# Performance work log

Hardware: AMD Instinct MI355X
Metric: run time of the kernel (lower is better)

Reference implementation:

```python
import jax, jax.numpy as jnp
import numpy as np
from jax import lax

B, D, H, FF, M = 256, 256, 8, 1024, 2048
HD = D // H
SCALE = 1.0 / np.sqrt(HD).astype(np.float32)
THR, MOM, LR = 0.5, 0.9, 0.1


def setup_inputs() -> dict:
    key = jax.random.key(0)
    ks = jax.random.split(key, 8)
    w = lambda k, sh: jax.random.normal(k, sh, dtype=jnp.float32) * 0.02
    return {
        "src": jax.random.normal(ks[0], (B, D), dtype=jnp.float32),
        "memory": jax.random.normal(ks[1], (M, D), dtype=jnp.float32) * 0.1,
        "momentum": jnp.zeros((M, D), jnp.float32),
        "scores": jax.random.uniform(ks[2], (M,), dtype=jnp.float32),
        "in_proj_w": w(ks[3], (3 * D, D)), "in_proj_b": jnp.zeros((3 * D,), jnp.float32),
        "out_w": w(ks[4], (D, D)), "out_b": jnp.zeros((D,), jnp.float32),
        "w1": w(ks[5], (FF, D)), "b1": jnp.zeros((FF,), jnp.float32),
        "w2": w(ks[6], (D, FF)), "b2": jnp.zeros((D,), jnp.float32),
        "g1": jnp.ones((D,), jnp.float32), "be1": jnp.zeros((D,), jnp.float32),
        "g2": jnp.ones((D,), jnp.float32), "be2": jnp.zeros((D,), jnp.float32),
        "ptr": M,
    }


def _ln(x, g, b):
    m = x.mean(-1, keepdims=True)
    v = ((x - m) ** 2).mean(-1, keepdims=True)
    return (x - m) / jnp.sqrt(v + 1e-5) * g + b


def reference(src, memory, momentum, scores, in_proj_w, in_proj_b, out_w, out_b,
              w1, b1, w2, b2, g1, be1, g2, be2, ptr):
    # --- surprise: 1 - max cosine similarity to memory slots ---
    xn = src / jnp.maximum(jnp.linalg.norm(src, axis=-1, keepdims=True), 1e-8)
    mn = memory / jnp.maximum(jnp.linalg.norm(memory, axis=-1, keepdims=True), 1e-8)
    sims = xn @ mn.T                                    # [B, M]
    surprises = jnp.where(jnp.linalg.norm(memory) == 0.0,
                          jnp.ones((B,), src.dtype), 1.0 - sims.max(-1))
    # --- self-attention; only the last (src) query row is used ---
    Wq, Wk, Wv = jnp.split(in_proj_w, 3, axis=0)
    bq, bk, bv = jnp.split(in_proj_b, 3, axis=0)
    q = (src @ Wq.T + bq).reshape(B, H, HD)             # [B,H,HD]
    k_mem = (memory @ Wk.T + bk).reshape(M, H, HD)      # shared across batch
    v_mem = (memory @ Wv.T + bv).reshape(M, H, HD)
    k_src = (src @ Wk.T + bk).reshape(B, H, HD)
    v_src = (src @ Wv.T + bv).reshape(B, H, HD)
    logits_mem = jnp.einsum('bhd,mhd->bhm', q, k_mem) * SCALE   # [B,H,M]
    logit_self = (q * k_src).sum(-1) * SCALE                    # [B,H]
    logits = jnp.concatenate([logits_mem, logit_self[..., None]], -1)  # [B,H,M+1]
    attn = jax.nn.softmax(logits, axis=-1)
    ctx = jnp.einsum('bhm,mhd->bhd', attn[..., :M], v_mem) + attn[..., M, None] * v_src
    attn_out = ctx.reshape(B, D) @ out_w.T + out_b
    h = _ln(src + attn_out, g1, be1)
    # --- sequential memory scatter update (detached in original) ---
    x_det = lax.stop_gradient(h)
    s_det = lax.stop_gradient(surprises)

    def step(carry, inp):
        mem, mom, sc, p = carry
        xi, si = inp
        cond = (si > THR) | (p < M)
        idx = jnp.mod(p, M)
        diff = xi - mem[idx]
        new_mom = MOM * mom[idx] + (1.0 - MOM) * diff
        mem = mem.at[idx].add(jnp.where(cond, LR * new_mom, 0.0))
        mom = mom.at[idx].set(jnp.where(cond, new_mom, mom[idx]))
        sc = sc.at[idx].set(jnp.where(cond, si, sc[idx]))
        return (mem, mom, sc, p + cond.astype(jnp.int32)), None

    (mem_f, mom_f, sc_f, _), _ = lax.scan(
        step, (memory, momentum, scores, jnp.int32(ptr)), (x_det, s_det))
    # --- FFN ---
    ff = jax.nn.relu(h @ w1.T + b1) @ w2.T + b2
    out = _ln(h + ff, g2, be2)
    return out, mem_f, mom_f, sc_f
```

## Files before the change

### kernel.cpp

```cpp
#include <hip/hip_runtime.h>
#include <math.h>

#define SCALE_F 0.17677669529663687f

typedef __attribute__((ext_vector_type(8))) short short8;
typedef __attribute__((ext_vector_type(4))) short short4v;
typedef __attribute__((ext_vector_type(4))) float f32x4;

__device__ inline short tobf(float x) {
    unsigned u = __float_as_uint(x);
    unsigned r = (u + 0x7FFFu + ((u >> 16) & 1u)) >> 16;
    return (short)r;
}
__device__ inline float frombf(short s) {
    return __uint_as_float(((unsigned)(unsigned short)s) << 16);
}

__global__ __launch_bounds__(256) void cvt2_k(
    const float* __restrict__ src, const float* __restrict__ memory,
    const float* __restrict__ ipw, const float* __restrict__ out_w,
    const float* __restrict__ w1, const float* __restrict__ w2,
    short* __restrict__ srcsplit, short* __restrict__ memsplit,
    short* __restrict__ ipw_bf, short* __restrict__ outw_bf,
    short* __restrict__ w1_bf, short* __restrict__ w2_bf,
    float* __restrict__ nx, float* __restrict__ nm, float* __restrict__ nm2)
{
    int j = blockIdx.x, t = threadIdx.x, w = t >> 6, l = t & 63;
    if (j < 576) {
        int r = j * 4 + w;
        bool issrc = r < 256;
        int rr = issrc ? r : r - 256;
        const float* rowp = issrc ? src + (long long)rr * 256 : memory + (long long)rr * 256;
        int c = l * 4;
        float4 x = *(const float4*)(rowp + c);
        short h0 = tobf(x.x), h1 = tobf(x.y), h2 = tobf(x.z), h3 = tobf(x.w);
        short4v hi4 = {h0, h1, h2, h3};
        short4v lo4 = {tobf(x.x - frombf(h0)), tobf(x.y - frombf(h1)),
                       tobf(x.z - frombf(h2)), tobf(x.w - frombf(h3))};
        long long b = (long long)rr * 768;
        if (issrc) {
            *(short4v*)&srcsplit[b + c] = hi4;
            *(short4v*)&srcsplit[b + 256 + c] = hi4;
            *(short4v*)&srcsplit[b + 512 + c] = lo4;
        } else {
            *(short4v*)&memsplit[b + c] = hi4;
            *(short4v*)&memsplit[b + 256 + c] = lo4;
            *(short4v*)&memsplit[b + 512 + c] = hi4;
        }
        float ss = x.x * x.x + x.y * x.y + x.z * x.z + x.w * x.w;
        #pragma unroll
        for (int m = 32; m; m >>= 1) ss += __shfl_xor(ss, m, 64);
        if (l == 0) {
            if (issrc) nx[rr] = fmaxf(sqrtf(ss), 1e-8f);
            else { nm[rr] = fmaxf(sqrtf(ss), 1e-8f); nm2[rr] = ss; }
        }
    } else {
        long long base = (long long)(j - 576) * 2048 + t * 8;
        const float* sp; short* dp; long long off;
        if (base < 196608)      { sp = ipw;   dp = ipw_bf;  off = base; }
        else if (base < 262144) { sp = out_w; dp = outw_bf; off = base - 196608; }
        else if (base < 524288) { sp = w1;    dp = w1_bf;   off = base - 262144; }
        else                    { sp = w2;    dp = w2_bf;   off = base - 524288; }
        float4 a = *(const float4*)(sp + off);
        float4 b4 = *(const float4*)(sp + off + 4);
        short8 o = {tobf(a.x), tobf(a.y), tobf(a.z), tobf(a.w),
                    tobf(b4.x), tobf(b4.y), tobf(b4.z), tobf(b4.w)};
        *(short8*)&dp[off] = o;
    }
}

__device__ __forceinline__ void gemm_tile(short* lds,
    const short* __restrict__ A, int lda, const short* __restrict__ B, int ldb,
    float* Cf, short* Cb, int ldc, long long coff, const float* bias,
    int M, int N, int Klen, int kbeg, float alpha, int relu, int transC, int bx, int by)
{
    short* Al = lds;
    short* Bl = lds + 2560;
    int t = threadIdx.x, w = t >> 6, l = t & 63;
    int r0 = by * 64, c0 = bx * 64;
    int srow = t >> 2, scol = (t & 3) * 8;
    f32x4 acc[4] = {{0.f,0.f,0.f,0.f},{0.f,0.f,0.f,0.f},{0.f,0.f,0.f,0.f},{0.f,0.f,0.f,0.f}};
    for (int kk = 0; kk < Klen; kk += 32) {
        int k0 = kbeg + kk;
        short8 va = {0,0,0,0,0,0,0,0};
        if (r0 + srow < M) va = *(const short8*)(A + (long long)(r0 + srow) * lda + k0 + scol);
        *(short8*)&Al[srow * 40 + scol] = va;
        short8 vb = {0,0,0,0,0,0,0,0};
        if (c0 + srow < N) vb = *(const short8*)(B + (long long)(c0 + srow) * ldb + k0 + scol);
        *(short8*)&Bl[srow * 40 + scol] = vb;
        __syncthreads();
        short8 af = *(const short8*)&Al[(w * 16 + (l & 15)) * 40 + (l >> 4) * 8];
        #pragma unroll
        for (int j = 0; j < 4; j++) {
            short8 bf = *(const short8*)&Bl[(j * 16 + (l & 15)) * 40 + (l >> 4) * 8];
            acc[j] = __builtin_amdgcn_mfma_f32_16x16x32_bf16(af, bf, acc[j], 0, 0, 0);
        }
        __syncthreads();
    }
    int lc = l & 15, lr = (l >> 4) * 4;
    #pragma unroll
    for (int j = 0; j < 4; j++) {
        int col = c0 + j * 16 + lc;
        if (col >= N) continue;
        float bv = bias ? bias[col] : 0.f;
        #pragma unroll
        for (int r = 0; r < 4; r++) {
            int row = r0 + w * 16 + lr + r;
            if (row >= M) continue;
            float v = acc[j][r] * alpha + bv;
            if (relu) v = fmaxf(v, 0.f);
            long long idx = coff + (transC ? (long long)col * ldc + row
                                           : (long long)row * ldc + col);
            if (Cf) Cf[idx] = v;
            else    Cb[idx] = tobf(v);
        }
    }
}

__global__ __launch_bounds__(256) void gemm4_k(
    const short* __restrict__ srcsplit, const short* __restrict__ memsplit,
    const short* __restrict__ ipw_bf, const float* __restrict__ ipb,
    float* __restrict__ simdot, short* __restrict__ qkv_bf,
    short* __restrict__ k_bf, short* __restrict__ vt_bf)
{
    __shared__ short lds[5120];
    int bid = blockIdx.x;
    const short *A, *B; const float *bias; float *Cf; short *Cb;
    int lda, ldb, ldc, M, N, K, transC, bx, by;
    if (bid < 128) {
        A = srcsplit; lda = 768; B = memsplit; ldb = 768;
        Cf = simdot; Cb = nullptr; ldc = 2048; bias = nullptr;
        M = 256; N = 2048; K = 768; transC = 0;
        bx = bid & 31; by = bid >> 5;
    } else if (bid < 256) {
        int r = bid - 128;
        A = memsplit + 512; lda = 768; B = ipw_bf + 65536; ldb = 256;
        Cf = nullptr; Cb = k_bf; ldc = 256; bias = ipb + 256;
        M = 2048; N = 256; K = 256; transC = 0;
        bx = r & 3; by = r >> 2;
    } else if (bid < 384) {
        int r = bid - 256;
        A = memsplit + 512; lda = 768; B = ipw_bf + 131072; ldb = 256;
        Cf = nullptr; Cb = vt_bf; ldc = 2048; bias = ipb + 512;
        M = 2048; N = 256; K = 256; transC = 1;
        bx = r & 3; by = r >> 2;
    } else {
        int r = bid - 384;
        A = srcsplit; lda = 768; B = ipw_bf; ldb = 256;
        Cf = nullptr; Cb = qkv_bf; ldc = 768; bias = ipb;
        M = 256; N = 768; K = 256; transC = 0;
        bx = r % 12; by = r / 12;
    }
    gemm_tile(lds, A, lda, B, ldb, Cf, Cb, ldc, 0, bias, M, N, K, 0, 1.f, 0, transC, bx, by);
}

__global__ __launch_bounds__(256) void flash_sur_k(
    const short* __restrict__ qkv_bf, const short* __restrict__ k_bf,
    const short* __restrict__ vt_bf,
    float* __restrict__ pvpart, float* __restrict__ mpart, float* __restrict__ lpart,
    const float* __restrict__ simdot, const float* __restrict__ nx,
    const float* __restrict__ nm, const float* __restrict__ nm2, float* __restrict__ sur)
{
    __shared__ __align__(16) short smem[29696];
    int bid = blockIdx.x;
    int t = threadIdx.x;
    if (bid >= 256) {
        float* red = (float*)smem;
        int b = bid - 256;
        float tot = 0.f;
        for (int m = t; m < 2048; m += 256) tot += nm2[m];
        red[t] = tot; __syncthreads();
        for (int s = 128; s; s >>= 1) { if (t < s) red[t] += red[t + s]; __syncthreads(); }
        float total = red[0];
        __syncthreads();
        float invx = 1.f / nx[b];
        float mx = -1e30f;
        for (int m = t; m < 2048; m += 256) {
            float s = simdot[(long long)b * 2048 + m] * invx / nm[m];
            mx = fmaxf(mx, s);
        }
        red[t] = mx; __syncthreads();
        for (int s = 128; s; s >>= 1) { if (t < s) red[t] = fmaxf(red[t], red[t + s]); __syncthreads(); }
        if (t == 0) sur[b] = (total == 0.f) ? 1.f : 1.f - red[0];
        return;
    }
    int ms = bid & 7, h = (bid >> 3) & 7, qt = bid >> 6;
    int q0 = qt * 64, m0 = ms * 256;
    int S = bid & 63;
    int w = t >> 6, l = t & 63;
    short* Ql = smem;
    short* Kl = smem + 2560;
    short* Pl = smem + 12800;
    { int srow = t >> 2, scol = (t & 3) * 8;
      *(short8*)&Ql[srow * 40 + scol] = *(const short8*)(qkv_bf + (q0 + srow) * 768 + h * 32 + scol); }
    #pragma unroll
    for (int s = 0; s < 4; s++) {
        int seg = t + s * 256; int row = seg >> 2, off = (seg & 3) * 8;
        *(short8*)&Kl[row * 40 + off] = *(const short8*)(k_bf + (long long)(m0 + row) * 256 + h * 32 + off);
    }
    __syncthreads();
    short8 af = *(const short8*)&Ql[(w * 16 + (l & 15)) * 40 + (l >> 4) * 8];
    f32x4 accL[16];
    #pragma unroll
    for (int j = 0; j < 16; j++) accL[j] = f32x4{0.f, 0.f, 0.f, 0.f};
    #pragma unroll
    for (int j = 0; j < 16; j++) {
        short8 bf = *(const short8*)&Kl[(j * 16 + (l & 15)) * 40 + (l >> 4) * 8];
        accL[j] = __builtin_amdgcn_mfma_f32_16x16x32_bf16(af, bf, accL[j], 0, 0, 0);
    }
    int r4 = (l >> 4) * 4;
    float mloc[4], lsum[4];
    #pragma unroll
    for (int r = 0; r < 4; r++) {
        float mx = -1e30f;
        #pragma unroll
        for (int j = 0; j < 16; j++) mx = fmaxf(mx, accL[j][r] * SCALE_F);
        #pragma unroll
        for (int msk = 1; msk < 16; msk <<= 1) mx = fmaxf(mx, __shfl_xor(mx, msk, 64));
        mloc[r] = mx;
    }
    #pragma unroll
    for (int j = 0; j < 16; j++)
        #pragma unroll
        for (int r = 0; r < 4; r++)
            accL[j][r] = __expf(accL[j][r] * SCALE_F - mloc[r]);
    #pragma unroll
    for (int r = 0; r < 4; r++) {
        float ls = 0.f;
        #pragma unroll
        for (int j = 0; j < 16; j++) ls += accL[j][r];
        #pragma unroll
        for (int msk = 1; msk < 16; msk <<= 1) ls += __shfl_xor(ls, msk, 64);
        lsum[r] = ls;
    }
    if ((l & 15) == 0) {
        #pragma unroll
        for (int r = 0; r < 4; r++) {
            int gq = q0 + w * 16 + r4 + r;
            mpart[S * 256 + gq] = mloc[r];
            lpart[S * 256 + gq] = lsum[r];
        }
    }
    #pragma unroll
    for (int j = 0; j < 16; j++)
        #pragma unroll
        for (int r = 0; r < 4; r++)
            Pl[(w * 16 + r4 + r) * 264 + j * 16 + (l & 15)] = tobf(accL[j][r]);
    __syncthreads();
    f32x4 accP[2] = {{0.f,0.f,0.f,0.f},{0.f,0.f,0.f,0.f}};
    #pragma unroll
    for (int ks = 0; ks < 8; ks++) {
        short8 pa = *(const short8*)&Pl[(w * 16 + (l & 15)) * 264 + ks * 32 + (l >> 4) * 8];
        #pragma unroll
        for (int df = 0; df < 2; df++) {
            short8 vb = *(const short8*)(vt_bf + (long long)(h * 32 + df * 16 + (l & 15)) * 2048
                                         + m0 + ks * 32 + (l >> 4) * 8);
            accP[df] = __builtin_amdgcn_mfma_f32_16x16x32_bf16(pa, vb, accP[df], 0, 0, 0);
        }
    }
    #pragma unroll
    for (int df = 0; df < 2; df++)
        #pragma unroll
        for (int r = 0; r < 4; r++) {
            int gq = q0 + w * 16 + r4 + r;
            pvpart[((long long)S * 256 + gq) * 32 + df * 16 + (l & 15)] = accP[df][r];
        }
}

__global__ __launch_bounds__(256) void attn_gemm_k(
    const short* __restrict__ qkv_bf, const float* __restrict__ mpart,
    const float* __restrict__ lpart, const float* __restrict__ pvpart,
    const short* __restrict__ outw_bf, float* __restrict__ attn_part,
    const float* __restrict__ sur, const int* __restrict__ ptr, int* __restrict__ inv)
{
    __shared__ float ws_n[64][8];
    __shared__ float es_n[64];
    __shared__ short Al[2560];
    __shared__ short Bl[2560];
    int j = blockIdx.x, t = threadIdx.x;
    if (j >= 128) {
        int* ired = (int*)ws_n;
        for (int m = t; m < 2048; m += 256) inv[m] = -1;
        float s = sur[t];
        int p0 = ptr[0];
        int thresh = 2048 - p0;
        bool cond = (t < thresh) || (s > 0.5f);
        unsigned long long ball = __ballot(cond);
        int lane = t & 63, wv = t >> 6;
        if (lane == 0) ired[wv] = __popcll(ball);
        __syncthreads();
        int off = 0;
        for (int i = 0; i < wv; i++) off += ired[i];
        int rank = off + __popcll(ball & ((1ULL << lane) - 1ULL));
        if (cond) inv[(p0 + rank) & 2047] = t;
        return;
    }
    int h = j >> 4, r = j & 15, bx = r & 3, by = r >> 2;
    int b0 = by * 64, c0 = bx * 64;
    #pragma unroll
    for (int p = 0; p < 8; p++) {
        int rl = p * 8 + (t >> 5);
        int lane32 = t & 31;
        int b = b0 + rl;
        float q = frombf(qkv_bf[b * 768 + h * 32 + lane32]);
        float k = frombf(qkv_bf[b * 768 + 256 + h * 32 + lane32]);
        float prod = q * k;
        #pragma unroll
        for (int m = 16; m; m >>= 1) prod += __shfl_xor(prod, m, 64);
        float sl = prod * SCALE_F;
        if (lane32 < 8) {
            int S = h * 8 + lane32;
            float msv = mpart[S * 256 + b];
            float lpv = lpart[S * 256 + b];
            float mx = msv;
            #pragma unroll
            for (int m = 4; m; m >>= 1) mx = fmaxf(mx, __shfl_xor(mx, m, 64));
            float Mf = fmaxf(mx, sl);
            float wgt = __expf(msv - Mf);
            float suml = wgt * lpv;
            #pragma unroll
            for (int m = 4; m; m >>= 1) suml += __shfl_xor(suml, m, 64);
            float Es = __expf(sl - Mf);
            float Ls = suml + Es;
            ws_n[rl][lane32] = wgt / Ls;
            if (lane32 == 0) es_n[rl] = Es / Ls;
        }
    }
    __syncthreads();
    {
        int rl = t >> 2, cg = (t & 3) * 8;
        int b = b0 + rl;
        short8 vs8 = *(const short8*)(qkv_bf + b * 768 + 512 + h * 32 + cg);
        float es = es_n[rl];
        float a8[8];
        #pragma unroll
        for (int d = 0; d < 8; d++) a8[d] = es * frombf(vs8[d]);
        #pragma unroll
        for (int s = 0; s < 8; s++) {
            float wn = ws_n[rl][s];
            const float* pvb = pvpart + ((long long)(h * 8 + s) * 256 + b) * 32 + cg;
            float4 p0 = *(const float4*)pvb;
            float4 p1 = *(const float4*)(pvb + 4);
            a8[0] += wn * p0.x; a8[1] += wn * p0.y; a8[2] += wn * p0.z; a8[3] += wn * p0.w;
            a8[4] += wn * p1.x; a8[5] += wn * p1.y; a8[6] += wn * p1.z; a8[7] += wn * p1.w;
        }
        short8 o = {tobf(a8[0]), tobf(a8[1]), tobf(a8[2]), tobf(a8[3]),
                    tobf(a8[4]), tobf(a8[5]), tobf(a8[6]), tobf(a8[7])};
        *(short8*)&Al[rl * 40 + cg] = o;
        *(short8*)&Bl[rl * 40 + cg] = *(const short8*)(outw_bf + (long long)(c0 + rl) * 256 + h * 32 + cg);
    }
    __syncthreads();
    int w = t >> 6, l = t & 63;
    short8 af = *(const short8*)&Al[(w * 16 + (l & 15)) * 40 + (l >> 4) * 8];
    f32x4 acc[4] = {{0.f,0.f,0.f,0.f},{0.f,0.f,0.f,0.f},{0.f,0.f,0.f,0.f},{0.f,0.f,0.f,0.f}};
    #pragma unroll
    for (int j4 = 0; j4 < 4; j4++) {
        short8 bf = *(const short8*)&Bl[(j4 * 16 + (l & 15)) * 40 + (l >> 4) * 8];
        acc[j4] = __builtin_amdgcn_mfma_f32_16x16x32_bf16(af, bf, acc[j4], 0, 0, 0);
    }
    int lc = l & 15, lr = (l >> 4) * 4;
    #pragma unroll
    for (int j4 = 0; j4 < 4; j4++) {
        int col = c0 + j4 * 16 + lc;
        #pragma unroll
        for (int rr = 0; rr < 4; rr++) {
            int row = b0 + w * 16 + lr + rr;
            attn_part[(long long)h * 65536 + row * 256 + col] = acc[j4][rr];
        }
    }
}

__global__ __launch_bounds__(256) void ff1_ln_k(
    const float* __restrict__ attn_part, const float* __restrict__ out_b,
    const float* __restrict__ src, const float* __restrict__ g1,
    const float* __restrict__ be1, const short* __restrict__ w1_bf,
    const float* __restrict__ b1, float* __restrict__ hbuf, short* __restrict__ ff1_bf)
{
    __shared__ short Afull[64 * 264];
    __shared__ short Bl[2560];
    int bx = blockIdx.x, by = blockIdx.y;
    int t = threadIdx.x, w = t >> 6, l = t & 63;
    #pragma unroll
    for (int p = 0; p < 16; p++) {
        int rl = p * 4 + w;
        int r = by * 64 + rl;
        int c = l * 4;
        float4 x = *(const float4*)(out_b + c);
        float4 sv = *(const float4*)(src + (long long)r * 256 + c);
        x.x += sv.x; x.y += sv.y; x.z += sv.z; x.w += sv.w;
        #pragma unroll
        for (int pp = 0; pp < 8; pp++) {
            float4 a = *(const float4*)(attn_part + (long long)pp * 65536 + r * 256 + c);
            x.x += a.x; x.y += a.y; x.z += a.z; x.w += a.w;
        }
        float s = x.x + x.y + x.z + x.w;
        #pragma unroll
        for (int m = 32; m; m >>= 1) s += __shfl_xor(s, m, 64);
        float mean = s * (1.f / 256.f);
        float4 cv = {x.x - mean, x.y - mean, x.z - mean, x.w - mean};
        float ss = cv.x * cv.x + cv.y * cv.y + cv.z * cv.z + cv.w * cv.w;
        #pragma unroll
        for (int m = 32; m; m >>= 1) ss += __shfl_xor(ss, m, 64);
        float rstd = rsqrtf(ss * (1.f / 256.f) + 1e-5f);
        float4 gg = *(const float4*)(g1 + c);
        float4 bb = *(const float4*)(be1 + c);
        float4 y = {cv.x * rstd * gg.x + bb.x, cv.y * rstd * gg.y + bb.y,
                    cv.z * rstd * gg.z + bb.z, cv.w * rstd * gg.w + bb.w};
        if (bx == 0) *(float4*)(hbuf + (long long)r * 256 + c) = y;
        short4v yb = {tobf(y.x), tobf(y.y), tobf(y.z), tobf(y.w)};
        *(short4v*)&Afull[rl * 264 + c] = yb;
    }
    __syncthreads();
    int c0 = bx * 64;
    int srow = t >> 2, scol = (t & 3) * 8;
    f32x4 acc[4] = {{0.f,0.f,0.f,0.f},{0.f,0.f,0.f,0.f},{0.f,0.f,0.f,0.f},{0.f,0.f,0.f,0.f}};
    for (int kk = 0; kk < 256; kk += 32) {
        *(short8*)&Bl[srow * 40 + scol] = *(const short8*)(w1_bf + (long long)(c0 + srow) * 256 + kk + scol);
        __syncthreads();
        short8 af = *(const short8*)&Afull[(w * 16 + (l & 15)) * 264 + kk + (l >> 4) * 8];
        #pragma unroll
        for (int j = 0; j < 4; j++) {
            short8 bf = *(const short8*)&Bl[(j * 16 + (l & 15)) * 40 + (l >> 4) * 8];
            acc[j] = __builtin_amdgcn_mfma_f32_16x16x32_bf16(af, bf, acc[j], 0, 0, 0);
        }
        __syncthreads();
    }
    int lc = l & 15, lr = (l >> 4) * 4;
    #pragma unroll
    for (int j = 0; j < 4; j++) {
        int col = c0 + j * 16 + lc;
        float bv = b1[col];
        #pragma unroll
        for (int r = 0; r < 4; r++) {
            int row = by * 64 + w * 16 + lr + r;
            float v = fmaxf(acc[j][r] + bv, 0.f);
            ff1_bf[(long long)row * 1024 + col] = tobf(v);
        }
    }
}

__global__ __launch_bounds__(256) void ff2_mem_k(
    const short* __restrict__ ff1_bf, const short* __restrict__ w2_bf,
    float* __restrict__ ff2_part,
    const float* __restrict__ memory, const float* __restrict__ momentum,
    const float* __restrict__ scores, const float* __restrict__ hbuf,
    const float* __restrict__ sur, const int* __restrict__ inv,
    float* __restrict__ mem_o, float* __restrict__ mom_o, float* __restrict__ sc_o)
{
    __shared__ short lds[5120];
    int j = blockIdx.x, t = threadIdx.x;
    if (j < 128) {
        int ks = j >> 4, r = j & 15, bx = r & 3, by = r >> 2;
        gemm_tile(lds, ff1_bf, 1024, w2_bf, 1024, ff2_part, nullptr, 256,
                  (long long)ks * 65536, nullptr, 256, 256, 128, ks * 128, 1.f, 0, 0, bx, by);
        return;
    }
    int w = t >> 6, l = t & 63;
    int m = (j - 128) * 4 + w;
    int b = inv[m];
    long long o = (long long)m * 256 + l * 4;
    float4 xm = *(const float4*)(memory + o);
    float4 mo = *(const float4*)(momentum + o);
    if (b >= 0) {
        float4 hb = *(const float4*)(hbuf + (long long)b * 256 + l * 4);
        float4 nmom = {0.9f * mo.x + 0.1f * (hb.x - xm.x), 0.9f * mo.y + 0.1f * (hb.y - xm.y),
                       0.9f * mo.z + 0.1f * (hb.z - xm.z), 0.9f * mo.w + 0.1f * (hb.w - xm.w)};
        float4 nm4 = {xm.x + 0.1f * nmom.x, xm.y + 0.1f * nmom.y,
                      xm.z + 0.1f * nmom.z, xm.w + 0.1f * nmom.w};
        *(float4*)(mem_o + o) = nm4;
        *(float4*)(mom_o + o) = nmom;
        if (l == 0) sc_o[m] = sur[b];
    } else {
        *(float4*)(mem_o + o) = xm;
        *(float4*)(mom_o + o) = mo;
        if (l == 0) sc_o[m] = scores[m];
    }
}

__global__ __launch_bounds__(256) void ln2_k(
    const float* __restrict__ ff2_part, const float* __restrict__ b2,
    const float* __restrict__ hbuf, const float* __restrict__ g2,
    const float* __restrict__ be2, float* __restrict__ out_main)
{
    int t = threadIdx.x, w = t >> 6, l = t & 63;
    int r = blockIdx.x * 4 + w;
    int c = l * 4;
    float4 x = *(const float4*)(b2 + c);
    float4 hv = *(const float4*)(hbuf + (long long)r * 256 + c);
    x.x += hv.x; x.y += hv.y; x.z += hv.z; x.w += hv.w;
    #pragma unroll
    for (int pp = 0; pp < 8; pp++) {
        float4 a = *(const float4*)(ff2_part + (long long)pp * 65536 + r * 256 + c);
        x.x += a.x; x.y += a.y; x.z += a.z; x.w += a.w;
    }
    float s = x.x + x.y + x.z + x.w;
    #pragma unroll
    for (int m = 32; m; m >>= 1) s += __shfl_xor(s, m, 64);
    float mean = s * (1.f / 256.f);
    float4 cv = {x.x - mean, x.y - mean, x.z - mean, x.w - mean};
    float ss = cv.x * cv.x + cv.y * cv.y + cv.z * cv.z + cv.w * cv.w;
    #pragma unroll
    for (int m = 32; m; m >>= 1) ss += __shfl_xor(ss, m, 64);
    float rstd = rsqrtf(ss * (1.f / 256.f) + 1e-5f);
    float4 gg = *(const float4*)(g2 + c);
    float4 bb = *(const float4*)(be2 + c);
    float4 y = {cv.x * rstd * gg.x + bb.x, cv.y * rstd * gg.y + bb.y,
                cv.z * rstd * gg.z + bb.z, cv.w * rstd * gg.w + bb.w};
    *(float4*)(out_main + (long long)r * 256 + c) = y;
}

extern "C" void kernel_launch(void* const* d_in, const int* in_sizes, int n_in,
                              void* d_out, int out_size, void* d_ws, size_t ws_size,
                              hipStream_t stream)
{
    const float* src      = (const float*)d_in[0];
    const float* memory   = (const float*)d_in[1];
    const float* momentum = (const float*)d_in[2];
    const float* scores   = (const float*)d_in[3];
    const float* ipw      = (const float*)d_in[4];
    const float* ipb      = (const float*)d_in[5];
    const float* out_w    = (const float*)d_in[6];
    const float* out_b    = (const float*)d_in[7];
    const float* w1       = (const float*)d_in[8];
    const float* b1       = (const float*)d_in[9];
    const float* w2       = (const float*)d_in[10];
    const float* b2       = (const float*)d_in[11];
    const float* g1       = (const float*)d_in[12];
    const float* be1      = (const float*)d_in[13];
    const float* g2       = (const float*)d_in[14];
    const float* be2      = (const float*)d_in[15];
    const int*   ptr      = (const int*)d_in[16];

    float* o = (float*)d_out;
    float* out_main = o;
    float* mem_o = o + 65536;
    float* mom_o = mem_o + 524288;
    float* sc_o  = mom_o + 524288;

    char* wp = (char*)d_ws;
    auto alloc = [&](size_t n) { void* q = (void*)wp; wp += (n + 255) & ~(size_t)255; return q; };
    short* srcsplit = (short*)alloc(393216);
    short* memsplit = (short*)alloc(3145728);
    short* ipw_bf   = (short*)alloc(393216);
    short* outw_bf  = (short*)alloc(131072);
    short* w1_bf    = (short*)alloc(524288);
    short* w2_bf    = (short*)alloc(524288);
    short* qkv_bf   = (short*)alloc(393216);
    short* k_bf     = (short*)alloc(1048576);
    short* vt_bf    = (short*)alloc(1048576);
    short* ff1_bf   = (short*)alloc(524288);
    float* simdot   = (float*)alloc(2097152);
    float* pvpart   = (float*)alloc(2097152);
    float* mpart    = (float*)alloc(65536);
    float* lpart    = (float*)alloc(65536);
    float* attn_part= (float*)alloc(2097152);
    float* ff2_part = (float*)alloc(2097152);
    float* hbuf     = (float*)alloc(262144);
    float* nx       = (float*)alloc(1024);
    float* nm       = (float*)alloc(8192);
    float* nm2      = (float*)alloc(8192);
    float* sur      = (float*)alloc(1024);
    int*   inv      = (int*)alloc(8192);

    cvt2_k<<<960, 256, 0, stream>>>(src, memory, ipw, out_w, w1, w2,
        srcsplit, memsplit, ipw_bf, outw_bf, w1_bf, w2_bf, nx, nm, nm2);
    gemm4_k<<<432, 256, 0, stream>>>(srcsplit, memsplit, ipw_bf, ipb,
        simdot, qkv_bf, k_bf, vt_bf);
    flash_sur_k<<<512, 256, 0, stream>>>(qkv_bf, k_bf, vt_bf, pvpart, mpart, lpart,
        simdot, nx, nm, nm2, sur);
    attn_gemm_k<<<129, 256, 0, stream>>>(qkv_bf, mpart, lpart, pvpart, outw_bf,
        attn_part, sur, ptr, inv);
    ff1_ln_k<<<dim3(16, 4), 256, 0, stream>>>(attn_part, out_b, src, g1, be1,
        w1_bf, b1, hbuf, ff1_bf);
    ff2_mem_k<<<640, 256, 0, stream>>>(ff1_bf, w2_bf, ff2_part,
        memory, momentum, scores, hbuf, sur, inv, mem_o, mom_o, sc_o);
    ln2_k<<<64, 256, 0, stream>>>(ff2_part, b2, hbuf, g2, be2, out_main);
}
```

Before: 155.0 us.

## Fuse bf16 conversion into projection GEMMs and split similarity into three partial products

Removes the separate conversion kernel. The projection GEMMs now load fp32 inputs and convert them to bf16 (hi or lo split) on the fly while staging into LDS. The three-term hi/lo similarity product becomes three independent K=256 GEMM tiles whose partial results the surprise reduction sums, instead of one K=768 GEMM over pre-split buffers. The attention kernel also loads K in two halves into smaller LDS and reads Q fragments directly from global memory. This saves a launch and the intermediate buffer round trips, but conversion work is repeated across tiles and the fp32 partial-product writes triple.

```diff
diff --git a/kernel.cpp b/kernel.cpp
--- a/kernel.cpp
+++ b/kernel.cpp
@@ -16,63 +16,22 @@
     return __uint_as_float(((unsigned)(unsigned short)s) << 16);
 }
 
-__global__ __launch_bounds__(256) void cvt2_k(
-    const float* __restrict__ src, const float* __restrict__ memory,
-    const float* __restrict__ ipw, const float* __restrict__ out_w,
-    const float* __restrict__ w1, const float* __restrict__ w2,
-    short* __restrict__ srcsplit, short* __restrict__ memsplit,
-    short* __restrict__ ipw_bf, short* __restrict__ outw_bf,
-    short* __restrict__ w1_bf, short* __restrict__ w2_bf,
-    float* __restrict__ nx, float* __restrict__ nm, float* __restrict__ nm2)
-{
-    int j = blockIdx.x, t = threadIdx.x, w = t >> 6, l = t & 63;
-    if (j < 576) {
-        int r = j * 4 + w;
-        bool issrc = r < 256;
-        int rr = issrc ? r : r - 256;
-        const float* rowp = issrc ? src + (long long)rr * 256 : memory + (long long)rr * 256;
-        int c = l * 4;
-        float4 x = *(const float4*)(rowp + c);
-        short h0 = tobf(x.x), h1 = tobf(x.y), h2 = tobf(x.z), h3 = tobf(x.w);
-        short4v hi4 = {h0, h1, h2, h3};
-        short4v lo4 = {tobf(x.x - frombf(h0)), tobf(x.y - frombf(h1)),
-                       tobf(x.z - frombf(h2)), tobf(x.w - frombf(h3))};
-        long long b = (long long)rr * 768;
-        if (issrc) {
-            *(short4v*)&srcsplit[b + c] = hi4;
-            *(short4v*)&srcsplit[b + 256 + c] = hi4;
-            *(short4v*)&srcsplit[b + 512 + c] = lo4;
-        } else {
-            *(short4v*)&memsplit[b + c] = hi4;
-            *(short4v*)&memsplit[b + 256 + c] = lo4;
-            *(short4v*)&memsplit[b + 512 + c] = hi4;
-        }
-        float ss = x.x * x.x + x.y * x.y + x.z * x.z + x.w * x.w;
-        #pragma unroll
-        for (int m = 32; m; m >>= 1) ss += __shfl_xor(ss, m, 64);
-        if (l == 0) {
-            if (issrc) nx[rr] = fmaxf(sqrtf(ss), 1e-8f);
-            else { nm[rr] = fmaxf(sqrtf(ss), 1e-8f); nm2[rr] = ss; }
-        }
-    } else {
-        long long base = (long long)(j - 576) * 2048 + t * 8;
-        const float* sp; short* dp; long long off;
-        if (base < 196608)      { sp = ipw;   dp = ipw_bf;  off = base; }
-        else if (base < 262144) { sp = out_w; dp = outw_bf; off = base - 196608; }
-        else if (base < 524288) { sp = w1;    dp = w1_bf;   off = base - 262144; }
-        else                    { sp = w2;    dp = w2_bf;   off = base - 524288; }
-        float4 a = *(const float4*)(sp + off);
-        float4 b4 = *(const float4*)(sp + off + 4);
-        short8 o = {tobf(a.x), tobf(a.y), tobf(a.z), tobf(a.w),
-                    tobf(b4.x), tobf(b4.y), tobf(b4.z), tobf(b4.w)};
-        *(short8*)&dp[off] = o;
-    }
-}
-
-__device__ __forceinline__ void gemm_tile(short* lds,
-    const short* __restrict__ A, int lda, const short* __restrict__ B, int ldb,
-    float* Cf, short* Cb, int ldc, long long coff, const float* bias,
-    int M, int N, int Klen, int kbeg, float alpha, int relu, int transC, int bx, int by)
+__device__ __forceinline__ short8 cv8(const float* __restrict__ p, int lo) {
+    float4 a = *(const float4*)p, b = *(const float4*)(p + 4);
+    float xs[8] = {a.x, a.y, a.z, a.w, b.x, b.y, b.z, b.w};
+    short8 o;
+    #pragma unroll
+    for (int i = 0; i < 8; i++) {
+        short hi = tobf(xs[i]);
+        o[i] = lo ? tobf(xs[i] - frombf(hi)) : hi;
+    }
+    return o;
+}
+
+__device__ __forceinline__ void gemm_cv(short* lds,
+    const float* __restrict__ A, int lda, int aLo,
+    const float* __restrict__ B, int ldb, int bLo,
+    float* Cf, short* Cb, int ldc, const float* bias, int transC, int bx, int by)
 {
     short* Al = lds;
     short* Bl = lds + 2560;
@@ -80,14 +39,9 @@
     int r0 = by * 64, c0 = bx * 64;
     int srow = t >> 2, scol = (t & 3) * 8;
     f32x4 acc[4] = {{0.f,0.f,0.f,0.f},{0.f,0.f,0.f,0.f},{0.f,0.f,0.f,0.f},{0.f,0.f,0.f,0.f}};
-    for (int kk = 0; kk < Klen; kk += 32) {
-        int k0 = kbeg + kk;
-        short8 va = {0,0,0,0,0,0,0,0};
-        if (r0 + srow < M) va = *(const short8*)(A + (long long)(r0 + srow) * lda + k0 + scol);
-        *(short8*)&Al[srow * 40 + scol] = va;
-        short8 vb = {0,0,0,0,0,0,0,0};
-        if (c0 + srow < N) vb = *(const short8*)(B + (long long)(c0 + srow) * ldb + k0 + scol);
-        *(short8*)&Bl[srow * 40 + scol] = vb;
+    for (int kk = 0; kk < 256; kk += 32) {
+        *(short8*)&Al[srow * 40 + scol] = cv8(A + (long long)(r0 + srow) * lda + kk + scol, aLo);
+        *(short8*)&Bl[srow * 40 + scol] = cv8(B + (long long)(c0 + srow) * ldb + kk + scol, bLo);
         __syncthreads();
         short8 af = *(const short8*)&Al[(w * 16 + (l & 15)) * 40 + (l >> 4) * 8];
         #pragma unroll
@@ -101,69 +55,86 @@
     #pragma unroll
     for (int j = 0; j < 4; j++) {
         int col = c0 + j * 16 + lc;
-        if (col >= N) continue;
         float bv = bias ? bias[col] : 0.f;
         #pragma unroll
         for (int r = 0; r < 4; r++) {
             int row = r0 + w * 16 + lr + r;
-            if (row >= M) continue;
-            float v = acc[j][r] * alpha + bv;
-            if (relu) v = fmaxf(v, 0.f);
-            long long idx = coff + (transC ? (long long)col * ldc + row
-                                           : (long long)row * ldc + col);
+            float v = acc[j][r] + bv;
+            long long idx = transC ? (long long)col * ldc + row : (long long)row * ldc + col;
             if (Cf) Cf[idx] = v;
             else    Cb[idx] = tobf(v);
         }
     }
 }
 
-__global__ __launch_bounds__(256) void gemm4_k(
-    const short* __restrict__ srcsplit, const short* __restrict__ memsplit,
-    const short* __restrict__ ipw_bf, const float* __restrict__ ipb,
-    float* __restrict__ simdot, short* __restrict__ qkv_bf,
-    short* __restrict__ k_bf, short* __restrict__ vt_bf)
+__global__ __launch_bounds__(256) void proj_k(
+    const float* __restrict__ src, const float* __restrict__ memory,
+    const float* __restrict__ ipw, const float* __restrict__ ipb,
+    const float* __restrict__ out_w, const float* __restrict__ w1, const float* __restrict__ w2,
+    float* __restrict__ simdot_p, short* __restrict__ qkv_bf,
+    short* __restrict__ k_bf, short* __restrict__ vt_bf,
+    short* __restrict__ outw_bf, short* __restrict__ w1_bf, short* __restrict__ w2_bf,
+    float* __restrict__ nx, float* __restrict__ nm, float* __restrict__ nm2)
 {
     __shared__ short lds[5120];
-    int bid = blockIdx.x;
-    const short *A, *B; const float *bias; float *Cf; short *Cb;
-    int lda, ldb, ldc, M, N, K, transC, bx, by;
-    if (bid < 128) {
-        A = srcsplit; lda = 768; B = memsplit; ldb = 768;
-        Cf = simdot; Cb = nullptr; ldc = 2048; bias = nullptr;
-        M = 256; N = 2048; K = 768; transC = 0;
-        bx = bid & 31; by = bid >> 5;
-    } else if (bid < 256) {
-        int r = bid - 128;
-        A = memsplit + 512; lda = 768; B = ipw_bf + 65536; ldb = 256;
-        Cf = nullptr; Cb = k_bf; ldc = 256; bias = ipb + 256;
-        M = 2048; N = 256; K = 256; transC = 0;
-        bx = r & 3; by = r >> 2;
-    } else if (bid < 384) {
-        int r = bid - 256;
-        A = memsplit + 512; lda = 768; B = ipw_bf + 131072; ldb = 256;
-        Cf = nullptr; Cb = vt_bf; ldc = 2048; bias = ipb + 512;
-        M = 2048; N = 256; K = 256; transC = 1;
-        bx = r & 3; by = r >> 2;
+    int bid = blockIdx.x, t = threadIdx.x, w = t >> 6, l = t & 63;
+    if (bid < 384) {
+        int tm = bid >> 7, r = bid & 127;
+        int aLo = (tm == 2), bLo = (tm == 1);
+        gemm_cv(lds, src, 256, aLo, memory, 256, bLo,
+                simdot_p + (long long)tm * 524288, nullptr, 2048, nullptr, 0, r & 31, r >> 5);
+    } else if (bid < 512) {
+        int r = bid - 384;
+        gemm_cv(lds, memory, 256, 0, ipw + 65536, 256, 0,
+                nullptr, k_bf, 256, ipb + 256, 0, r & 3, r >> 2);
+    } else if (bid < 640) {
+        int r = bid - 512;
+        gemm_cv(lds, memory, 256, 0, ipw + 131072, 256, 0,
+                nullptr, vt_bf, 2048, ipb + 512, 1, r & 3, r >> 2);
+    } else if (bid < 688) {
+        int r = bid - 640;
+        gemm_cv(lds, src, 256, 0, ipw, 256, 0,
+                nullptr, qkv_bf, 768, ipb, 0, r % 12, r / 12);
+    } else if (bid < 724) {
+        int nb = bid - 688;
+        #pragma unroll
+        for (int i = 0; i < 16; i++) {
+            int r = nb * 64 + i * 4 + w;
+            bool issrc = r < 256;
+            int rr = issrc ? r : r - 256;
+            const float* rowp = issrc ? src + (long long)rr * 256 : memory + (long long)rr * 256;
+            float4 x = *(const float4*)(rowp + l * 4);
+            float ss = x.x * x.x + x.y * x.y + x.z * x.z + x.w * x.w;
+            #pragma unroll
+            for (int m = 32; m; m >>= 1) ss += __shfl_xor(ss, m, 64);
+            if (l == 0) {
+                if (issrc) nx[rr] = fmaxf(sqrtf(ss), 1e-8f);
+                else { nm[rr] = fmaxf(sqrtf(ss), 1e-8f); nm2[rr] = ss; }
+            }
+        }
     } else {
-        int r = bid - 384;
-        A = srcsplit; lda = 768; B = ipw_bf; ldb = 256;
-        Cf = nullptr; Cb = qkv_bf; ldc = 768; bias = ipb;
-        M = 256; N = 768; K = 256; transC = 0;
-        bx = r % 12; by = r / 12;
-    }
-    gemm_tile(lds, A, lda, B, ldb, Cf, Cb, ldc, 0, bias, M, N, K, 0, 1.f, 0, transC, bx, by);
+        long long base = (long long)(bid - 724) * 4096 + t * 8;
+        #pragma unroll
+        for (int rep = 0; rep < 2; rep++) {
+            long long e = base + rep * 2048;
+            const float* sp; short* dp; long long off;
+            if (e < 65536)       { sp = out_w; dp = outw_bf; off = e; }
+            else if (e < 327680) { sp = w1;    dp = w1_bf;   off = e - 65536; }
+            else                 { sp = w2;    dp = w2_bf;   off = e - 327680; }
+            *(short8*)&dp[off] = cv8(sp + off, 0);
+        }
+    }
 }
 
 __global__ __launch_bounds__(256) void flash_sur_k(
     const short* __restrict__ qkv_bf, const short* __restrict__ k_bf,
     const short* __restrict__ vt_bf,
     float* __restrict__ pvpart, float* __restrict__ mpart, float* __restrict__ lpart,
-    const float* __restrict__ simdot, const float* __restrict__ nx,
+    const float* __restrict__ simdot_p, const float* __restrict__ nx,
     const float* __restrict__ nm, const float* __restrict__ nm2, float* __restrict__ sur)
 {
-    __shared__ __align__(16) short smem[29696];
-    int bid = blockIdx.x;
-    int t = threadIdx.x;
+    __shared__ __align__(16) short smem[22016];
+    int bid = blockIdx.x, t = threadIdx.x;
     if (bid >= 256) {
         float* red = (float*)smem;
         int b = bid - 256;
@@ -176,8 +147,9 @@
         float invx = 1.f / nx[b];
         float mx = -1e30f;
         for (int m = t; m < 2048; m += 256) {
-            float s = simdot[(long long)b * 2048 + m] * invx / nm[m];
-            mx = fmaxf(mx, s);
+            long long i = (long long)b * 2048 + m;
+            float d = simdot_p[i] + simdot_p[524288 + i] + simdot_p[1048576 + i];
+            mx = fmaxf(mx, d * invx / nm[m]);
         }
         red[t] = mx; __syncthreads();
         for (int s = 128; s; s >>= 1) { if (t < s) red[t] = fmaxf(red[t], red[t + s]); __syncthreads(); }
@@ -188,25 +160,27 @@
     int q0 = qt * 64, m0 = ms * 256;
     int S = bid & 63;
     int w = t >> 6, l = t & 63;
-    short* Ql = smem;
-    short* Kl = smem + 2560;
-    short* Pl = smem + 12800;
-    { int srow = t >> 2, scol = (t & 3) * 8;
-      *(short8*)&Ql[srow * 40 + scol] = *(const short8*)(qkv_bf + (q0 + srow) * 768 + h * 32 + scol); }
-    #pragma unroll
-    for (int s = 0; s < 4; s++) {
-        int seg = t + s * 256; int row = seg >> 2, off = (seg & 3) * 8;
-        *(short8*)&Kl[row * 40 + off] = *(const short8*)(k_bf + (long long)(m0 + row) * 256 + h * 32 + off);
-    }
-    __syncthreads();
-    short8 af = *(const short8*)&Ql[(w * 16 + (l & 15)) * 40 + (l >> 4) * 8];
+    short* Kl = smem;
+    short* Pl = smem + 5120;
+    short8 af = *(const short8*)(qkv_bf + (q0 + w * 16 + (l & 15)) * 768 + h * 32 + (l >> 4) * 8);
     f32x4 accL[16];
     #pragma unroll
     for (int j = 0; j < 16; j++) accL[j] = f32x4{0.f, 0.f, 0.f, 0.f};
     #pragma unroll
-    for (int j = 0; j < 16; j++) {
-        short8 bf = *(const short8*)&Kl[(j * 16 + (l & 15)) * 40 + (l >> 4) * 8];
-        accL[j] = __builtin_amdgcn_mfma_f32_16x16x32_bf16(af, bf, accL[j], 0, 0, 0);
+    for (int half = 0; half < 2; half++) {
+        #pragma unroll
+        for (int s = 0; s < 2; s++) {
+            int seg = t + s * 256; int row = seg >> 2, off = (seg & 3) * 8;
+            *(short8*)&Kl[row * 40 + off] =
+                *(const short8*)(k_bf + (long long)(m0 + half * 128 + row) * 256 + h * 32 + off);
+        }
+        __syncthreads();
+        #pragma unroll
+        for (int j = 0; j < 8; j++) {
+            short8 bf = *(const short8*)&Kl[(j * 16 + (l & 15)) * 40 + (l >> 4) * 8];
+            accL[half * 8 + j] = __builtin_amdgcn_mfma_f32_16x16x32_bf16(af, bf, accL[half * 8 + j], 0, 0, 0);
+        }
+        __syncthreads();
     }
     int r4 = (l >> 4) * 4;
     float mloc[4], lsum[4];
@@ -439,6 +413,41 @@
     }
 }
 
+__device__ __forceinline__ void gemm_tile(short* lds,
+    const short* __restrict__ A, int lda, const short* __restrict__ B, int ldb,
+    float* Cf, int ldc, long long coff, int Klen, int kbeg, int bx, int by)
+{
+    short* Al = lds;
+    short* Bl = lds + 2560;
+    int t = threadIdx.x, w = t >> 6, l = t & 63;
+    int r0 = by * 64, c0 = bx * 64;
+    int srow = t >> 2, scol = (t & 3) * 8;
+    f32x4 acc[4] = {{0.f,0.f,0.f,0.f},{0.f,0.f,0.f,0.f},{0.f,0.f,0.f,0.f},{0.f,0.f,0.f,0.f}};
+    for (int kk = 0; kk < Klen; kk += 32) {
+        int k0 = kbeg + kk;
+        *(short8*)&Al[srow * 40 + scol] = *(const short8*)(A + (long long)(r0 + srow) * lda + k0 + scol);
+        *(short8*)&Bl[srow * 40 + scol] = *(const short8*)(B + (long long)(c0 + srow) * ldb + k0 + scol);
+        __syncthreads();
+        short8 af = *(const short8*)&Al[(w * 16 + (l & 15)) * 40 + (l >> 4) * 8];
+        #pragma unroll
+        for (int j = 0; j < 4; j++) {
+            short8 bf = *(const short8*)&Bl[(j * 16 + (l & 15)) * 40 + (l >> 4) * 8];
+            acc[j] = __builtin_amdgcn_mfma_f32_16x16x32_bf16(af, bf, acc[j], 0, 0, 0);
+        }
+        __syncthreads();
+    }
+    int lc = l & 15, lr = (l >> 4) * 4;
+    #pragma unroll
+    for (int j = 0; j < 4; j++) {
+        int col = c0 + j * 16 + lc;
+        #pragma unroll
+        for (int r = 0; r < 4; r++) {
+            int row = r0 + w * 16 + lr + r;
+            Cf[coff + (long long)row * ldc + col] = acc[j][r];
+        }
+    }
+}
+
 __global__ __launch_bounds__(256) void ff2_mem_k(
     const short* __restrict__ ff1_bf, const short* __restrict__ w2_bf,
     float* __restrict__ ff2_part,
@@ -450,9 +459,9 @@
     __shared__ short lds[5120];
     int j = blockIdx.x, t = threadIdx.x;
     if (j < 128) {
-        int ks = j >> 4, r = j & 15, bx = r & 3, by = r >> 2;
-        gemm_tile(lds, ff1_bf, 1024, w2_bf, 1024, ff2_part, nullptr, 256,
-                  (long long)ks * 65536, nullptr, 256, 256, 128, ks * 128, 1.f, 0, 0, bx, by);
+        int ks = j >> 4, r = j & 15;
+        gemm_tile(lds, ff1_bf, 1024, w2_bf, 1024, ff2_part, 256,
+                  (long long)ks * 65536, 128, ks * 128, r & 3, r >> 2);
         return;
     }
     int w = t >> 6, l = t & 63;
@@ -539,17 +548,14 @@
 
     char* wp = (char*)d_ws;
     auto alloc = [&](size_t n) { void* q = (void*)wp; wp += (n + 255) & ~(size_t)255; return q; };
-    short* srcsplit = (short*)alloc(393216);
-    short* memsplit = (short*)alloc(3145728);
-    short* ipw_bf   = (short*)alloc(393216);
+    short* qkv_bf   = (short*)alloc(393216);
+    short* k_bf     = (short*)alloc(1048576);
+    short* vt_bf    = (short*)alloc(1048576);
     short* outw_bf  = (short*)alloc(131072);
     short* w1_bf    = (short*)alloc(524288);
     short* w2_bf    = (short*)alloc(524288);
-    short* qkv_bf   = (short*)alloc(393216);
-    short* k_bf     = (short*)alloc(1048576);
-    short* vt_bf    = (short*)alloc(1048576);
     short* ff1_bf   = (short*)alloc(524288);
-    float* simdot   = (float*)alloc(2097152);
+    float* simdot_p = (float*)alloc(6291456);
     float* pvpart   = (float*)alloc(2097152);
     float* mpart    = (float*)alloc(65536);
     float* lpart    = (float*)alloc(65536);
@@ -562,12 +568,10 @@
     float* sur      = (float*)alloc(1024);
     int*   inv      = (int*)alloc(8192);
 
-    cvt2_k<<<960, 256, 0, stream>>>(src, memory, ipw, out_w, w1, w2,
-        srcsplit, memsplit, ipw_bf, outw_bf, w1_bf, w2_bf, nx, nm, nm2);
-    gemm4_k<<<432, 256, 0, stream>>>(srcsplit, memsplit, ipw_bf, ipb,
-        simdot, qkv_bf, k_bf, vt_bf);
+    proj_k<<<868, 256, 0, stream>>>(src, memory, ipw, ipb, out_w, w1, w2,
+        simdot_p, qkv_bf, k_bf, vt_bf, outw_bf, w1_bf, w2_bf, nx, nm, nm2);
     flash_sur_k<<<512, 256, 0, stream>>>(qkv_bf, k_bf, vt_bf, pvpart, mpart, lpart,
-        simdot, nx, nm, nm2, sur);
+        simdot_p, nx, nm, nm2, sur);
     attn_gemm_k<<<129, 256, 0, stream>>>(qkv_bf, mpart, lpart, pvpart, outw_bf,
         attn_part, sur, ptr, inv);
     ff1_ln_k<<<dim3(16, 4), 256, 0, stream>>>(attn_part, out_b, src, g1, be1,
```

Result: faster. 145.9 us (-5.8%).
